# Kernel tuning notes

Measured on AMD Instinct MI355X. Metric: run time of the kernel, lower is better.

Reference implementation:

```python
import jax, jax.numpy as jnp
import numpy as np

N_NODES = 100000
N_EDGES = 1600000
N_FEAT = 64
HIDDEN = 16


def setup_inputs() -> dict:
    key = jax.random.key(0)
    ks = jax.random.split(key, 10)
    x = jax.random.normal(ks[0], (N_NODES, N_FEAT), dtype=jnp.float32)
    edge_index = jax.random.randint(ks[1], (2, N_EDGES), 0, N_NODES, dtype=jnp.int64)
    As = jax.random.normal(ks[2], (2, N_EDGES), dtype=jnp.float32)
    ws_weights = jax.random.normal(ks[3], (2,), dtype=jnp.float32)
    Wl1 = jax.random.normal(ks[4], (N_FEAT, HIDDEN), dtype=jnp.float32) / np.sqrt(N_FEAT)
    bl1 = jnp.zeros((HIDDEN,), dtype=jnp.float32)
    Wr1 = jax.random.normal(ks[5], (N_FEAT, HIDDEN), dtype=jnp.float32) / np.sqrt(N_FEAT)
    Wl2 = jax.random.normal(ks[6], (HIDDEN, 1), dtype=jnp.float32) / np.sqrt(HIDDEN)
    bl2 = jnp.zeros((1,), dtype=jnp.float32)
    Wr2 = jax.random.normal(ks[7], (HIDDEN, 1), dtype=jnp.float32) / np.sqrt(HIDDEN)
    return {"x": x, "edge_index": edge_index, "As": As, "ws_weights": ws_weights,
            "Wl1": Wl1, "bl1": bl1, "Wr1": Wr1, "Wl2": Wl2, "bl2": bl2, "Wr2": Wr2}


def reference(x, edge_index, As, ws_weights, Wl1, bl1, Wr1, Wl2, bl2, Wr2):
    # WeightedSumLayer: weighted sum of per-edge weight vectors
    ewm = jnp.einsum('m,me->e', ws_weights, As)  # [E]
    # edge mask (nonzero weighted sum keeps the edge); instead of slicing to a
    # data-dependent edge count, zero out masked messages (same aggregation).
    mask = (ewm != 0).astype(x.dtype)  # [E]
    src, dst = edge_index[0], edge_index[1]
    n = x.shape[0]

    # SAGEConv layer 1 (aggr='sum'): out = lin_l(sum_j x_j) + lin_r(x)
    msg1 = x[src] * mask[:, None]                             # [E, F]
    agg1 = jax.ops.segment_sum(msg1, dst, num_segments=n)     # [N, F]
    h = jax.nn.relu(agg1 @ Wl1 + bl1 + x @ Wr1)               # [N, H]

    # SAGEConv layer 2
    msg2 = h[src] * mask[:, None]                             # [E, H]
    agg2 = jax.ops.segment_sum(msg2, dst, num_segments=n)     # [N, H]
    out = agg2 @ Wl2 + bl2 + h @ Wr2                          # [N, 1]
    return out
```

## Files before the change

kernel.cpp:

```cpp
#include <hip/hip_runtime.h>
#include <hip/hip_bf16.h>

constexpr int NN = 100000;
constexpr int NE = 1600000;
constexpr int NF = 64;
constexpr int NH = 16;

constexpr int NPB  = 128;
constexpr int LB   = 7;
constexpr int NBKT = (NN + NPB - 1) / NPB;
constexpr int CAP  = 2560;
constexpr int TB   = 512;
constexpr int CHUNK = 8192;
constexpr int NBF   = (NE + CHUNK - 1) / CHUNK;
constexpr int NGT   = (NN + TB - 1) / TB;
constexpr int FD = NBKT + 1;

constexpr int SMEM_BYTES = CHUNK * 2 + NBKT * 4 + FD * 4 + 32;

__device__ __forceinline__ float bf16_to_f32(unsigned short u) {
    return __uint_as_float(((unsigned int)u) << 16);
}
__device__ __forceinline__ unsigned short f32_to_bf16(float f) {
    __hip_bfloat16 hb = __float2bfloat16(f);
    return *reinterpret_cast<unsigned short*>(&hb);
}

__global__ __launch_bounds__(TB)
void k_fused(const float* __restrict__ x,
             const float* __restrict__ Wl1,
             const float* __restrict__ Wr1,
             unsigned short* __restrict__ p,
             float* __restrict__ r,
             const int* __restrict__ ei, const float* __restrict__ As,
             const float* __restrict__ ws,
             unsigned int* __restrict__ gchunk, int* __restrict__ fdirT)
{
    __shared__ __align__(16) char smem[SMEM_BYTES];
    int b    = blockIdx.x;
    int role = (b < NBF) ? 1 : 0;
    int rb   = role ? b : b - NBF;
    int tid  = threadIdx.x;

    if (role == 0) {
        float* sW = (float*)smem;
        for (int i = tid; i < NF * NH; i += TB) {
            sW[i]           = Wl1[i];
            sW[NF * NH + i] = Wr1[i];
        }
        __syncthreads();

        int n = rb * TB + tid;
        if (n >= NN) return;

        float aL[NH], aR[NH];
#pragma unroll
        for (int j = 0; j < NH; ++j) { aL[j] = 0.f; aR[j] = 0.f; }

        const float4* xr = reinterpret_cast<const float4*>(x + (size_t)n * NF);
#pragma unroll
        for (int k4 = 0; k4 < NF / 4; ++k4) {
            float4 v = xr[k4];
            float xs[4] = {v.x, v.y, v.z, v.w};
#pragma unroll
            for (int t2 = 0; t2 < 4; ++t2) {
                const float* wl = &sW[(k4 * 4 + t2) * NH];
                const float* wr = &sW[NF * NH + (k4 * 4 + t2) * NH];
#pragma unroll
                for (int j = 0; j < NH; ++j) {
                    aL[j] = fmaf(xs[t2], wl[j], aL[j]);
                    aR[j] = fmaf(xs[t2], wr[j], aR[j]);
                }
            }
        }

        unsigned int pu[8];
#pragma unroll
        for (int j2 = 0; j2 < 8; ++j2)
            pu[j2] = (unsigned int)f32_to_bf16(aL[2*j2]) |
                     ((unsigned int)f32_to_bf16(aL[2*j2+1]) << 16);
        uint4* pp = reinterpret_cast<uint4*>(p + (size_t)n * NH);
        pp[0] = make_uint4(pu[0], pu[1], pu[2], pu[3]);
        pp[1] = make_uint4(pu[4], pu[5], pu[6], pu[7]);

        float4* rp = reinterpret_cast<float4*>(r + (size_t)n * NH);
#pragma unroll
        for (int j4 = 0; j4 < NH / 4; ++j4)
            rp[j4] = make_float4(aR[j4*4], aR[j4*4+1], aR[j4*4+2], aR[j4*4+3]);
    } else {
        unsigned short* srk  = (unsigned short*)smem;
        int* lcnt  = (int*)(smem + CHUNK * 2);
        int* fscan = lcnt + NBKT;
        int* wsum  = fscan + FD;

        for (int i = tid; i < NBKT; i += TB) lcnt[i] = 0;
        __syncthreads();

        int base = rb * CHUNK;
        float w0 = ws[0], w1 = ws[1];

#pragma unroll
        for (int j = 0; j < CHUNK / TB; ++j) {
            int idx = j * TB + tid;
            int e = base + idx;
            unsigned short rk = 0xFFFFu;
            if (e < NE) {
                float ewm = w0 * As[e] + w1 * As[NE + e];
                if (ewm != 0.f)
                    rk = (unsigned short)atomicAdd(&lcnt[ei[NE + e] >> LB], 1);
            }
            srk[idx] = rk;
        }
        __syncthreads();

        {
            int loc[2]; int s0 = 0;
#pragma unroll
            for (int g = 0; g < 2; ++g) {
                int idx = tid * 2 + g;
                int v = (idx < NBKT) ? lcnt[idx] : 0;
                loc[g] = s0; s0 += v;
            }
            int lane = tid & 63, w = tid >> 6;
            int si = s0;
#pragma unroll
            for (int off = 1; off < 64; off <<= 1) {
                int u = __shfl_up(si, off);
                if (lane >= off) si += u;
            }
            if (lane == 63) wsum[w] = si;
            __syncthreads();
            int bse = 0;
            for (int i = 0; i < w; ++i) bse += wsum[i];
            int excl = bse + si - s0;
#pragma unroll
            for (int g = 0; g < 2; ++g) {
                int idx = tid * 2 + g;
                if (idx < NBKT) fscan[idx] = excl + loc[g];
            }
            if (tid == TB - 1) fscan[NBKT] = bse + si;
        }
        __syncthreads();

        for (int i = tid; i < FD; i += TB)
            fdirT[(size_t)i * NBF + rb] = fscan[i];

#pragma unroll
        for (int j = 0; j < CHUNK / TB; ++j) {
            int idx = j * TB + tid;
            unsigned short rk = srk[idx];
            if (rk != 0xFFFFu) {
                int e   = base + idx;
                int dst = ei[NE + e];
                int bk  = dst >> LB;
                gchunk[(size_t)rb * CHUNK + fscan[bk] + rk] =
                    ((unsigned)ei[e] << LB) | (unsigned)(dst & (NPB - 1));
            }
        }
    }
}

__global__ __launch_bounds__(512)
void k_agg1(const int* __restrict__ fdirT, const unsigned int* __restrict__ gchunk,
            unsigned int* __restrict__ bmem,
            const unsigned short* __restrict__ p, const float* __restrict__ r,
            const float* __restrict__ bl1, const float* __restrict__ Wl2,
            const float* __restrict__ bl2, const float* __restrict__ Wr2,
            float* __restrict__ q, float* __restrict__ out,
            int* __restrict__ gsoff)
{
    __shared__ unsigned int sbm[CAP];
    __shared__ unsigned int ssorted[CAP];
    __shared__ int fstart[NBF];
    __shared__ int foff[NBF + 1];
    __shared__ int hist[NPB];
    __shared__ int soff[NPB + 1];
    __shared__ int wsum8[8];

    int b = blockIdx.x;
    int tid = threadIdx.x;
    if (tid < NPB) hist[tid] = 0;

    {
        int sz = 0;
        if (tid < NBF) {
            int s0 = fdirT[(size_t)b * NBF + tid];
            int s1 = fdirT[(size_t)(b + 1) * NBF + tid];
            fstart[tid] = s0;
            sz = s1 - s0;
        }
        int lane = tid & 63, w = tid >> 6;
        int si = sz;
#pragma unroll
        for (int off = 1; off < 64; off <<= 1) {
            int u = __shfl_up(si, off);
            if (lane >= off) si += u;
        }
        if (lane == 63) wsum8[w] = si;
        __syncthreads();
        int bse = 0;
        for (int i = 0; i < w; ++i) bse += wsum8[i];
        if (tid < NBF) foff[tid] = bse + si - sz;
        if (tid == 511) foff[NBF] = bse + si;
    }
    __syncthreads();

    int cnt = min(foff[NBF], CAP);

    {
        int grp = tid >> 4, k = tid & 15;
        for (int f = grp; f < NBF; f += 32) {
            int o  = foff[f];
            int sz = foff[f + 1] - o;
            int s  = fstart[f];
            const unsigned int* src = gchunk + (size_t)f * CHUNK + s;
            int lim = min(sz, CAP - o);
            for (int j = k; j < lim; j += 16)
                sbm[o + j] = src[j];
        }
    }
    __syncthreads();

    int rk[CAP / 512];
#pragma unroll
    for (int j = 0; j < CAP / 512; ++j) {
        int i = j * 512 + tid;
        if (i < cnt)
            rk[j] = atomicAdd(&hist[sbm[i] & (NPB - 1)], 1);
    }
    __syncthreads();

    {
        int v = (tid < NPB) ? hist[tid] : 0;
        int lane = tid & 63, w = tid >> 6;
        int si = v;
#pragma unroll
        for (int off = 1; off < 64; off <<= 1) {
            int u = __shfl_up(si, off);
            if (lane >= off) si += u;
        }
        if (lane == 63) wsum8[w] = si;
        __syncthreads();
        int bse = 0;
        for (int i = 0; i < w; ++i) bse += wsum8[i];
        if (tid < NPB) soff[tid + 1] = bse + si;
        if (tid == 0) soff[0] = 0;
    }
    __syncthreads();

#pragma unroll
    for (int j = 0; j < CAP / 512; ++j) {
        int i = j * 512 + tid;
        if (i < cnt) {
            unsigned int w = sbm[i];
            ssorted[soff[w & (NPB - 1)] + rk[j]] = w;
        }
    }
    __syncthreads();

    for (int i = tid; i < cnt; i += 512)
        bmem[(size_t)b * CAP + i] = ssorted[i];
    if (tid < NPB + 1)
        gsoff[(size_t)b * (NPB + 1) + tid] = soff[tid];

    int g = tid >> 4, k = tid & 15;
    int n0 = b * NPB;
#pragma unroll
    for (int jj = 0; jj < 4; ++jj) {
        int nl = g * 4 + jj;
        int s = soff[nl], e = soff[nl + 1];
        float a = 0.f;
        int i = s;
        for (; i + 3 < e; i += 4) {
            unsigned w0 = ssorted[i], w1 = ssorted[i+1], w2 = ssorted[i+2], w3 = ssorted[i+3];
            float v0 = bf16_to_f32(p[(size_t)(w0 >> LB) * NH + k]);
            float v1 = bf16_to_f32(p[(size_t)(w1 >> LB) * NH + k]);
            float v2 = bf16_to_f32(p[(size_t)(w2 >> LB) * NH + k]);
            float v3 = bf16_to_f32(p[(size_t)(w3 >> LB) * NH + k]);
            a += (v0 + v1) + (v2 + v3);
        }
        for (; i < e; ++i)
            a += bf16_to_f32(p[(size_t)(ssorted[i] >> LB) * NH + k]);

        int n = n0 + nl;
        if (n < NN) {
            float h = a + r[(size_t)n * NH + k] + bl1[k];
            h = h > 0.f ? h : 0.f;
            float qv = h * Wl2[k];
            float sv = h * Wr2[k];
#pragma unroll
            for (int m = 8; m >= 1; m >>= 1) {
                qv += __shfl_xor(qv, m);
                sv += __shfl_xor(sv, m);
            }
            if (k == 0) {
                q[n]   = qv;
                out[n] = sv + bl2[0];
            }
        }
    }
}

__global__ __launch_bounds__(256)
void k_agg2(const int* __restrict__ gsoff, const unsigned int* __restrict__ bmem,
            const float* __restrict__ q, float* __restrict__ out)
{
    int t = blockIdx.x * 256 + threadIdx.x;
    int n = t >> 2;
    int sub = t & 3;
    if (n >= NN) return;
    int b  = n >> LB;
    int dl = n & (NPB - 1);
    int s = gsoff[(size_t)b * (NPB + 1) + dl];
    int e = gsoff[(size_t)b * (NPB + 1) + dl + 1];
    const unsigned int* bm = bmem + (size_t)b * CAP;

    float a = 0.f;
    for (int i = s + sub; i < e; i += 4)
        a += q[bm[i] >> LB];
    a += __shfl_xor(a, 1);
    a += __shfl_xor(a, 2);
    if (sub == 0) out[n] += a;
}

extern "C" void kernel_launch(void* const* d_in, const int* in_sizes, int n_in,
                              void* d_out, int out_size, void* d_ws, size_t ws_size,
                              hipStream_t stream)
{
    const float* x   = (const float*)d_in[0];
    const int*   ei  = (const int*)  d_in[1];
    const float* As  = (const float*)d_in[2];
    const float* ws  = (const float*)d_in[3];
    const float* Wl1 = (const float*)d_in[4];
    const float* bl1 = (const float*)d_in[5];
    const float* Wr1 = (const float*)d_in[6];
    const float* Wl2 = (const float*)d_in[7];
    const float* bl2 = (const float*)d_in[8];
    const float* Wr2 = (const float*)d_in[9];
    float* out = (float*)d_out;

    unsigned short* p      = (unsigned short*)d_ws;
    float*          r      = (float*)(p + (size_t)NN * NH);
    float*          q      = r + (size_t)NN * NH;
    int*            gsoff  = (int*)(q + NN);
    int*            fdirT  = gsoff + (size_t)NBKT * (NPB + 1);
    unsigned int*   gchunk = (unsigned int*)(fdirT + (size_t)FD * NBF);
    unsigned int*   bmem   = gchunk + (size_t)NBF * CHUNK;

    int nblk = NBF + NGT;
    k_fused<<<nblk, TB, 0, stream>>>(x, Wl1, Wr1, p, r, ei, As, ws, gchunk, fdirT);
    k_agg1<<<NBKT, 512, 0, stream>>>(fdirT, gchunk, bmem, p, r, bl1, Wl2, bl2, Wr2,
                                     q, out, gsoff);
    k_agg2<<<(NN * 4 + 255) / 256, 256, 0, stream>>>(gsoff, bmem, q, out);
}
```

Baseline: 155.7 us.

## Cache edge payloads in LDS during bucketing and vectorize bf16 gather in agg1

The bucketing pass now builds the packed src/dst payload and bucket id once and keeps them in shared memory. Ranks are assigned with a second round of LDS atomics in the scatter pass, so edge_index is not read from global memory a second time. In k_agg1 each thread gathers a 32-bit word holding two bf16 features instead of one 16-bit value, halving the gather instruction count and the shuffle reduction depth. The cost is a larger LDS footprint in k_fused, which may reduce occupancy, plus extra LDS atomics that make the scatter order within a bucket nondeterministic.

```diff
diff --git a/kernel.cpp b/kernel.cpp
--- a/kernel.cpp
+++ b/kernel.cpp
@@ -16,7 +16,7 @@
 constexpr int NGT   = (NN + TB - 1) / TB;
 constexpr int FD = NBKT + 1;
 
-constexpr int SMEM_BYTES = CHUNK * 2 + NBKT * 4 + FD * 4 + 32;
+constexpr int SMEM_BYTES = CHUNK * 4 + CHUNK * 2 + NBKT * 4 + FD * 4 + 32;
 
 __device__ __forceinline__ float bf16_to_f32(unsigned short u) {
     return __uint_as_float(((unsigned int)u) << 16);
@@ -88,8 +88,9 @@
         for (int j4 = 0; j4 < NH / 4; ++j4)
             rp[j4] = make_float4(aR[j4*4], aR[j4*4+1], aR[j4*4+2], aR[j4*4+3]);
     } else {
-        unsigned short* srk  = (unsigned short*)smem;
-        int* lcnt  = (int*)(smem + CHUNK * 2);
+        unsigned int*   spay = (unsigned int*)smem;
+        unsigned short* sbk  = (unsigned short*)(smem + CHUNK * 4);
+        int* lcnt  = (int*)(smem + CHUNK * 6);
         int* fscan = lcnt + NBKT;
         int* wsum  = fscan + FD;
 
@@ -103,13 +104,20 @@
         for (int j = 0; j < CHUNK / TB; ++j) {
             int idx = j * TB + tid;
             int e = base + idx;
-            unsigned short rk = 0xFFFFu;
+            unsigned pay = 0xFFFFFFFFu;
+            unsigned short bk = 0;
             if (e < NE) {
                 float ewm = w0 * As[e] + w1 * As[NE + e];
-                if (ewm != 0.f)
-                    rk = (unsigned short)atomicAdd(&lcnt[ei[NE + e] >> LB], 1);
-            }
-            srk[idx] = rk;
+                if (ewm != 0.f) {
+                    int dst = ei[NE + e];
+                    int src = ei[e];
+                    bk  = (unsigned short)(dst >> LB);
+                    pay = ((unsigned)src << LB) | (unsigned)(dst & (NPB - 1));
+                    atomicAdd(&lcnt[bk], 1);
+                }
+            }
+            spay[idx] = pay;
+            sbk[idx]  = bk;
         }
         __syncthreads();
 
@@ -130,6 +138,7 @@
             }
             if (lane == 63) wsum[w] = si;
             __syncthreads();
+            for (int i = tid; i < NBKT; i += TB) lcnt[i] = 0;
             int bse = 0;
             for (int i = 0; i < w; ++i) bse += wsum[i];
             int excl = bse + si - s0;
@@ -148,13 +157,11 @@
 #pragma unroll
         for (int j = 0; j < CHUNK / TB; ++j) {
             int idx = j * TB + tid;
-            unsigned short rk = srk[idx];
-            if (rk != 0xFFFFu) {
-                int e   = base + idx;
-                int dst = ei[NE + e];
-                int bk  = dst >> LB;
-                gchunk[(size_t)rb * CHUNK + fscan[bk] + rk] =
-                    ((unsigned)ei[e] << LB) | (unsigned)(dst & (NPB - 1));
+            unsigned pay = spay[idx];
+            if (pay != 0xFFFFFFFFu) {
+                int bk = sbk[idx];
+                int rk = atomicAdd(&lcnt[bk], 1);
+                gchunk[(size_t)rb * CHUNK + fscan[bk] + rk] = pay;
             }
         }
     }
@@ -263,37 +270,45 @@
     if (tid < NPB + 1)
         gsoff[(size_t)b * (NPB + 1) + tid] = soff[tid];
 
-    int g = tid >> 4, k = tid & 15;
+    const unsigned int* pw = reinterpret_cast<const unsigned int*>(p);
+    const float2* r2 = reinterpret_cast<const float2*>(r);
+    int g = tid >> 3, m = tid & 7;
     int n0 = b * NPB;
 #pragma unroll
-    for (int jj = 0; jj < 4; ++jj) {
-        int nl = g * 4 + jj;
+    for (int jj = 0; jj < 2; ++jj) {
+        int nl = g * 2 + jj;
         int s = soff[nl], e = soff[nl + 1];
-        float a = 0.f;
+        float a0 = 0.f, a1 = 0.f;
         int i = s;
         for (; i + 3 < e; i += 4) {
             unsigned w0 = ssorted[i], w1 = ssorted[i+1], w2 = ssorted[i+2], w3 = ssorted[i+3];
-            float v0 = bf16_to_f32(p[(size_t)(w0 >> LB) * NH + k]);
-            float v1 = bf16_to_f32(p[(size_t)(w1 >> LB) * NH + k]);
-            float v2 = bf16_to_f32(p[(size_t)(w2 >> LB) * NH + k]);
-            float v3 = bf16_to_f32(p[(size_t)(w3 >> LB) * NH + k]);
-            a += (v0 + v1) + (v2 + v3);
-        }
-        for (; i < e; ++i)
-            a += bf16_to_f32(p[(size_t)(ssorted[i] >> LB) * NH + k]);
-
+            unsigned u0 = pw[(size_t)(w0 >> LB) * 8 + m];
+            unsigned u1 = pw[(size_t)(w1 >> LB) * 8 + m];
+            unsigned u2 = pw[(size_t)(w2 >> LB) * 8 + m];
+            unsigned u3 = pw[(size_t)(w3 >> LB) * 8 + m];
+            a0 += (__uint_as_float(u0 << 16) + __uint_as_float(u1 << 16))
+                + (__uint_as_float(u2 << 16) + __uint_as_float(u3 << 16));
+            a1 += (__uint_as_float(u0 & 0xFFFF0000u) + __uint_as_float(u1 & 0xFFFF0000u))
+                + (__uint_as_float(u2 & 0xFFFF0000u) + __uint_as_float(u3 & 0xFFFF0000u));
+        }
+        for (; i < e; ++i) {
+            unsigned u = pw[(size_t)(ssorted[i] >> LB) * 8 + m];
+            a0 += __uint_as_float(u << 16);
+            a1 += __uint_as_float(u & 0xFFFF0000u);
+        }
         int n = n0 + nl;
         if (n < NN) {
-            float h = a + r[(size_t)n * NH + k] + bl1[k];
-            h = h > 0.f ? h : 0.f;
-            float qv = h * Wl2[k];
-            float sv = h * Wr2[k];
-#pragma unroll
-            for (int m = 8; m >= 1; m >>= 1) {
-                qv += __shfl_xor(qv, m);
-                sv += __shfl_xor(sv, m);
-            }
-            if (k == 0) {
+            float2 rr = r2[(size_t)n * 8 + m];
+            float h0 = a0 + rr.x + bl1[2*m];
+            float h1 = a1 + rr.y + bl1[2*m+1];
+            h0 = h0 > 0.f ? h0 : 0.f;
+            h1 = h1 > 0.f ? h1 : 0.f;
+            float qv = h0 * Wl2[2*m] + h1 * Wl2[2*m+1];
+            float sv = h0 * Wr2[2*m] + h1 * Wr2[2*m+1];
+            qv += __shfl_xor(qv, 1); sv += __shfl_xor(sv, 1);
+            qv += __shfl_xor(qv, 2); sv += __shfl_xor(sv, 2);
+            qv += __shfl_xor(qv, 4); sv += __shfl_xor(sv, 4);
+            if (m == 0) {
                 q[n]   = qv;
                 out[n] = sv + bl2[0];
             }
```

Result: slower. 160.4 us (+3.0%).

## Replace per-bucket counting sort with shared-memory atomic accumulation in both aggregations

Applied to the files above, without the earlier changes.

Layer-1 aggregation no longer sorts the edges of each destination bucket with a histogram, a scan and a scatter. Each edge's gathered feature row is added straight into a per-bucket LDS accumulator with float atomics. Layer-2 aggregation likewise becomes one block per bucket that accumulates q values into LDS with atomics, using only a per-bucket count in place of per-node offsets. This removes the sort passes and several barriers, at the cost of LDS atomic contention and a summation order that is no longer deterministic.

```diff
diff --git a/kernel.cpp b/kernel.cpp
--- a/kernel.cpp
+++ b/kernel.cpp
@@ -162,24 +162,24 @@
 
 __global__ __launch_bounds__(512)
 void k_agg1(const int* __restrict__ fdirT, const unsigned int* __restrict__ gchunk,
-            unsigned int* __restrict__ bmem,
+            unsigned int* __restrict__ bmem, int* __restrict__ bcnt,
             const unsigned short* __restrict__ p, const float* __restrict__ r,
             const float* __restrict__ bl1, const float* __restrict__ Wl2,
             const float* __restrict__ bl2, const float* __restrict__ Wr2,
-            float* __restrict__ q, float* __restrict__ out,
-            int* __restrict__ gsoff)
+            float* __restrict__ q, float* __restrict__ out)
 {
     __shared__ unsigned int sbm[CAP];
-    __shared__ unsigned int ssorted[CAP];
+    __shared__ float sacc[NPB * NH];
     __shared__ int fstart[NBF];
     __shared__ int foff[NBF + 1];
-    __shared__ int hist[NPB];
-    __shared__ int soff[NPB + 1];
     __shared__ int wsum8[8];
 
     int b = blockIdx.x;
     int tid = threadIdx.x;
-    if (tid < NPB) hist[tid] = 0;
+
+#pragma unroll
+    for (int j = 0; j < NPB * NH / 512; ++j)
+        sacc[j * 512 + tid] = 0.f;
 
     {
         int sz = 0;
@@ -221,106 +221,90 @@
     }
     __syncthreads();
 
-    int rk[CAP / 512];
-#pragma unroll
-    for (int j = 0; j < CAP / 512; ++j) {
-        int i = j * 512 + tid;
-        if (i < cnt)
-            rk[j] = atomicAdd(&hist[sbm[i] & (NPB - 1)], 1);
-    }
-    __syncthreads();
+    for (int i = tid; i < cnt; i += 512)
+        bmem[(size_t)b * CAP + i] = sbm[i];
+    if (tid == 0) bcnt[b] = cnt;
 
     {
-        int v = (tid < NPB) ? hist[tid] : 0;
-        int lane = tid & 63, w = tid >> 6;
-        int si = v;
-#pragma unroll
-        for (int off = 1; off < 64; off <<= 1) {
-            int u = __shfl_up(si, off);
-            if (lane >= off) si += u;
-        }
-        if (lane == 63) wsum8[w] = si;
-        __syncthreads();
-        int bse = 0;
-        for (int i = 0; i < w; ++i) bse += wsum8[i];
-        if (tid < NPB) soff[tid + 1] = bse + si;
-        if (tid == 0) soff[0] = 0;
-    }
-    __syncthreads();
-
-#pragma unroll
-    for (int j = 0; j < CAP / 512; ++j) {
-        int i = j * 512 + tid;
+        int grp = tid >> 4, k = tid & 15;
+        int i = grp;
+        for (; i + 32 < cnt; i += 64) {
+            unsigned wa = sbm[i];
+            unsigned wb = sbm[i + 32];
+            float va = bf16_to_f32(p[(size_t)(wa >> LB) * NH + k]);
+            float vb = bf16_to_f32(p[(size_t)(wb >> LB) * NH + k]);
+            unsafeAtomicAdd(&sacc[(wa & (NPB - 1)) * NH + k], va);
+            unsafeAtomicAdd(&sacc[(wb & (NPB - 1)) * NH + k], vb);
+        }
         if (i < cnt) {
-            unsigned int w = sbm[i];
-            ssorted[soff[w & (NPB - 1)] + rk[j]] = w;
-        }
-    }
-    __syncthreads();
-
-    for (int i = tid; i < cnt; i += 512)
-        bmem[(size_t)b * CAP + i] = ssorted[i];
-    if (tid < NPB + 1)
-        gsoff[(size_t)b * (NPB + 1) + tid] = soff[tid];
-
-    int g = tid >> 4, k = tid & 15;
-    int n0 = b * NPB;
-#pragma unroll
-    for (int jj = 0; jj < 4; ++jj) {
-        int nl = g * 4 + jj;
-        int s = soff[nl], e = soff[nl + 1];
-        float a = 0.f;
-        int i = s;
-        for (; i + 3 < e; i += 4) {
-            unsigned w0 = ssorted[i], w1 = ssorted[i+1], w2 = ssorted[i+2], w3 = ssorted[i+3];
-            float v0 = bf16_to_f32(p[(size_t)(w0 >> LB) * NH + k]);
-            float v1 = bf16_to_f32(p[(size_t)(w1 >> LB) * NH + k]);
-            float v2 = bf16_to_f32(p[(size_t)(w2 >> LB) * NH + k]);
-            float v3 = bf16_to_f32(p[(size_t)(w3 >> LB) * NH + k]);
-            a += (v0 + v1) + (v2 + v3);
-        }
-        for (; i < e; ++i)
-            a += bf16_to_f32(p[(size_t)(ssorted[i] >> LB) * NH + k]);
-
-        int n = n0 + nl;
-        if (n < NN) {
-            float h = a + r[(size_t)n * NH + k] + bl1[k];
-            h = h > 0.f ? h : 0.f;
-            float qv = h * Wl2[k];
-            float sv = h * Wr2[k];
-#pragma unroll
-            for (int m = 8; m >= 1; m >>= 1) {
-                qv += __shfl_xor(qv, m);
-                sv += __shfl_xor(sv, m);
-            }
-            if (k == 0) {
-                q[n]   = qv;
-                out[n] = sv + bl2[0];
-            }
-        }
-    }
-}
-
-__global__ __launch_bounds__(256)
-void k_agg2(const int* __restrict__ gsoff, const unsigned int* __restrict__ bmem,
+            unsigned wa = sbm[i];
+            float va = bf16_to_f32(p[(size_t)(wa >> LB) * NH + k]);
+            unsafeAtomicAdd(&sacc[(wa & (NPB - 1)) * NH + k], va);
+        }
+    }
+    __syncthreads();
+
+    {
+        int g = tid >> 4, k = tid & 15;
+        int n0 = b * NPB;
+#pragma unroll
+        for (int jj = 0; jj < 4; ++jj) {
+            int nl = g * 4 + jj;
+            int n = n0 + nl;
+            if (n < NN) {
+                float h = sacc[nl * NH + k] + r[(size_t)n * NH + k] + bl1[k];
+                h = h > 0.f ? h : 0.f;
+                float qv = h * Wl2[k];
+                float sv = h * Wr2[k];
+#pragma unroll
+                for (int m = 8; m >= 1; m >>= 1) {
+                    qv += __shfl_xor(qv, m);
+                    sv += __shfl_xor(sv, m);
+                }
+                if (k == 0) {
+                    q[n]   = qv;
+                    out[n] = sv + bl2[0];
+                }
+            }
+        }
+    }
+}
+
+__global__ __launch_bounds__(512)
+void k_agg2(const unsigned int* __restrict__ bmem, const int* __restrict__ bcnt,
             const float* __restrict__ q, float* __restrict__ out)
 {
-    int t = blockIdx.x * 256 + threadIdx.x;
-    int n = t >> 2;
-    int sub = t & 3;
-    if (n >= NN) return;
-    int b  = n >> LB;
-    int dl = n & (NPB - 1);
-    int s = gsoff[(size_t)b * (NPB + 1) + dl];
-    int e = gsoff[(size_t)b * (NPB + 1) + dl + 1];
+    __shared__ float sacc2[NPB];
+    __shared__ int scnt;
+
+    int b = blockIdx.x;
+    int tid = threadIdx.x;
+    if (tid == 0) scnt = bcnt[b];
+    if (tid < NPB) sacc2[tid] = 0.f;
+    __syncthreads();
+
+    int cnt = scnt;
     const unsigned int* bm = bmem + (size_t)b * CAP;
 
-    float a = 0.f;
-    for (int i = s + sub; i < e; i += 4)
-        a += q[bm[i] >> LB];
-    a += __shfl_xor(a, 1);
-    a += __shfl_xor(a, 2);
-    if (sub == 0) out[n] += a;
+    int i = tid;
+    for (; i + 512 < cnt; i += 1024) {
+        unsigned wa = bm[i];
+        unsigned wb = bm[i + 512];
+        float va = q[wa >> LB];
+        float vb = q[wb >> LB];
+        unsafeAtomicAdd(&sacc2[wa & (NPB - 1)], va);
+        unsafeAtomicAdd(&sacc2[wb & (NPB - 1)], vb);
+    }
+    if (i < cnt) {
+        unsigned wa = bm[i];
+        unsafeAtomicAdd(&sacc2[wa & (NPB - 1)], q[wa >> LB]);
+    }
+    __syncthreads();
+
+    if (tid < NPB) {
+        int n = b * NPB + tid;
+        if (n < NN) out[n] += sacc2[tid];
+    }
 }
 
 extern "C" void kernel_launch(void* const* d_in, const int* in_sizes, int n_in,
@@ -342,14 +326,14 @@
     unsigned short* p      = (unsigned short*)d_ws;
     float*          r      = (float*)(p + (size_t)NN * NH);
     float*          q      = r + (size_t)NN * NH;
-    int*            gsoff  = (int*)(q + NN);
-    int*            fdirT  = gsoff + (size_t)NBKT * (NPB + 1);
+    int*            bcnt   = (int*)(q + NN);
+    int*            fdirT  = bcnt + NBKT;
     unsigned int*   gchunk = (unsigned int*)(fdirT + (size_t)FD * NBF);
     unsigned int*   bmem   = gchunk + (size_t)NBF * CHUNK;
 
     int nblk = NBF + NGT;
     k_fused<<<nblk, TB, 0, stream>>>(x, Wl1, Wr1, p, r, ei, As, ws, gchunk, fdirT);
-    k_agg1<<<NBKT, 512, 0, stream>>>(fdirT, gchunk, bmem, p, r, bl1, Wl2, bl2, Wr2,
-                                     q, out, gsoff);
-    k_agg2<<<(NN * 4 + 255) / 256, 256, 0, stream>>>(gsoff, bmem, q, out);
-}
+    k_agg1<<<NBKT, 512, 0, stream>>>(fdirT, gchunk, bmem, bcnt, p, r, bl1, Wl2,
+                                     bl2, Wr2, q, out);
+    k_agg2<<<NBKT, 512, 0, stream>>>(bmem, bcnt, q, out);
+}
```

Result: slower. 321.4 us (+106.4%).
